# Performance work log

Measured on AMD Instinct MI355X. Metric: run time of the kernel, lower is better.

Reference implementation:

```python
import jax, jax.numpy as jnp
import numpy as np

B, N, D, H, KS, DQ = 2048, 20, 512, 8, 3, 64
DK = D // H
LN_EPS = 1e-5


def _conv1d_same(x_bdn, w_oik):
    # x: [B, D, N], w: [O, I, K] -> [B, O, N], 'same' padding
    return jax.lax.conv_general_dilated(
        x_bdn, w_oik, window_strides=(1,), padding='SAME',
        dimension_numbers=('NCH', 'OIH', 'NCH'))


def _layernorm(x, g, b):
    m = jnp.mean(x, axis=-1, keepdims=True)
    v = jnp.var(x, axis=-1, keepdims=True)
    return (x - m) * jax.lax.rsqrt(v + LN_EPS) * g + b


def setup_inputs() -> dict:
    key = jax.random.key(0)
    ks = jax.random.split(key, 12)
    s = 0.02
    inp = {
        'x': jax.random.normal(ks[0], (B, N, D), dtype=jnp.float32),
        'Wq': jax.random.normal(ks[1], (D, D, KS), dtype=jnp.float32) * s,
        'Wk': jax.random.normal(ks[2], (D, D, KS), dtype=jnp.float32) * s,
        'Wv': jax.random.normal(ks[3], (D, D, KS), dtype=jnp.float32) * s,
        'gq_g': jnp.ones((D,), jnp.float32), 'gq_b': jnp.zeros((D,), jnp.float32),
        'gk_g': jnp.ones((D,), jnp.float32), 'gk_b': jnp.zeros((D,), jnp.float32),
        'gv_g': jnp.ones((D,), jnp.float32), 'gv_b': jnp.zeros((D,), jnp.float32),
        'rel_table': jax.random.normal(ks[4], (2 * N - 1, H), dtype=jnp.float32) * s,
        'gsb': jax.random.normal(ks[5], (H, N, N), dtype=jnp.float32) * s,
        'alpha': jnp.asarray(1.0, jnp.float32),
        'Wqf': jax.random.normal(ks[6], (D, DQ), dtype=jnp.float32) * s,
        'bqf': jnp.zeros((DQ,), jnp.float32),
        'Wqp': jax.random.normal(ks[7], (DQ, H), dtype=jnp.float32) * s,
        'bqp': jnp.zeros((H,), jnp.float32),
        'Wo': jax.random.normal(ks[8], (D, D), dtype=jnp.float32) * s,
        'bo': jnp.zeros((D,), jnp.float32),
    }
    return inp


def reference(x, Wq, Wk, Wv, gq_g, gq_b, gk_g, gk_b, gv_g, gv_b,
              rel_table, gsb, alpha, Wqf, bqf, Wqp, bqp, Wo, bo):
    xp = jnp.transpose(x, (0, 2, 1))  # [B, D, N]
    # conv QKV projections + LayerNorm + residual (use_conv_proj=True path)
    q = x + _layernorm(jnp.transpose(_conv1d_same(xp, Wq), (0, 2, 1)), gq_g, gq_b)
    k = x + _layernorm(jnp.transpose(_conv1d_same(xp, Wk), (0, 2, 1)), gk_g, gk_b)
    v = x + _layernorm(jnp.transpose(_conv1d_same(xp, Wv), (0, 2, 1)), gv_g, gv_b)
    # split heads: [B, H, N, DK]
    q = q.reshape(B, N, H, DK).transpose(0, 2, 1, 3)
    k = k.reshape(B, N, H, DK).transpose(0, 2, 1, 3)
    v = v.reshape(B, N, H, DK).transpose(0, 2, 1, 3)
    scale = 1.0 / jnp.sqrt(jnp.asarray(DK, jnp.float32))
    scores = jnp.einsum('bhnd,bhmd->bhnm', q, k) * scale  # [B, H, N, N]
    # relative positional bias over node index
    idx = jnp.arange(N)[:, None] - jnp.arange(N)[None, :] + N - 1  # [N, N]
    rel_bias = rel_table[idx]  # [N, N, H]
    scores = scores + jnp.transpose(rel_bias, (2, 0, 1))[None]
    # learned global spatial bias
    scores = scores + alpha * gsb[None]
    # dynamic adjacency bias from pairwise node features
    qf = jnp.tanh(x @ Wqf + bqf)  # [B, N, DQ]
    pair = qf[:, :, None, :] - qf[:, None, :, :]  # [B, N, N, DQ]
    dyn = pair @ Wqp + bqp  # [B, N, N, H]
    scores = scores + jnp.transpose(dyn, (0, 3, 1, 2))
    attn = jax.nn.softmax(scores, axis=-1)
    out = jnp.einsum('bhnm,bhmd->bhnd', attn, v)
    out = out.transpose(0, 2, 1, 3).reshape(B, N, D)
    return out @ Wo + bo
```

## Files before the change

kernel.cpp:

```cpp
#include <hip/hip_runtime.h>
#include <stdint.h>

#define Bn   2048
#define Nn   20
#define Dn   512
#define Hn   8
#define Mn   (Bn*Nn)
#define K3n  1536
#define NPn  22
#define BKn  32

typedef __attribute__((ext_vector_type(4))) float  floatx4;
typedef __attribute__((ext_vector_type(8))) __bf16 bf16x8;
typedef __attribute__((ext_vector_type(4))) __bf16 bf16x4;

__device__ __forceinline__ void gload_lds16(const void* g, void* l) {
  __builtin_amdgcn_global_load_lds(
      (const __attribute__((address_space(1))) void*)g,
      (__attribute__((address_space(3))) void*)l, 16, 0, 0);
}

__global__ void k_prep_xpad(const float* __restrict__ x, __bf16* __restrict__ xpad) {
  int idx = blockIdx.x * 256 + threadIdx.x;
  int d8 = idx & 63;
  int t  = idx >> 6;
  if (t >= Bn * NPn) return;
  int n = t % NPn;
  int b = t / NPn;
  bf16x8 v;
  if (n == 0 || n == NPn - 1) {
#pragma unroll
    for (int e = 0; e < 8; ++e) v[e] = (__bf16)0.f;
  } else {
    const float4 x0 = *(const float4*)(x + (size_t)((b * Nn + n - 1) * Dn) + d8 * 8);
    const float4 x1 = *(const float4*)(x + (size_t)((b * Nn + n - 1) * Dn) + d8 * 8 + 4);
    v[0] = (__bf16)x0.x; v[1] = (__bf16)x0.y; v[2] = (__bf16)x0.z; v[3] = (__bf16)x0.w;
    v[4] = (__bf16)x1.x; v[5] = (__bf16)x1.y; v[6] = (__bf16)x1.z; v[7] = (__bf16)x1.w;
  }
  *(bf16x8*)(xpad + (size_t)t * Dn + d8 * 8) = v;
}

__global__ void k_prep_wctf(const float* __restrict__ Wq, const float* __restrict__ Wk,
                            const float* __restrict__ Wv, __bf16* __restrict__ wctf) {
  int t = blockIdx.x * 256 + threadIdx.x;
  if (t >= 48 * 96 * 64) return;
  int l  = t & 63;
  int cb = (t >> 6) % 96;
  int kt = t / (96 * 64);
  int col = cb * 16 + (l & 15);
  int k   = kt * 32 + (l >> 4) * 8;
  int seg = col >> 9, o = col & 511;
  int kker = k >> 9, i = k & 511;
  const float* W = (seg == 0) ? Wq : ((seg == 1) ? Wk : Wv);
  const float* s = W + ((size_t)o * 512 + i) * 3 + kker;
  bf16x8 v;
#pragma unroll
  for (int e = 0; e < 8; ++e) v[e] = (__bf16)s[e * 3];
  *(bf16x8*)(wctf + (size_t)t * 8) = v;
}

__global__ void k_prep_wotf(const float* __restrict__ Wo, __bf16* __restrict__ wotf) {
  int t = blockIdx.x * 256 + threadIdx.x;
  if (t >= 16 * 32 * 64) return;
  int l  = t & 63;
  int cb = (t >> 6) & 31;
  int kt = t / (32 * 64);
  int col = cb * 16 + (l & 15);
  int k   = kt * 32 + (l >> 4) * 8;
  const float* s = Wo + (size_t)k * 512 + col;
  bf16x8 v;
#pragma unroll
  for (int e = 0; e < 8; ++e) v[e] = (__bf16)s[(size_t)e * 512];
  *(bf16x8*)(wotf + (size_t)t * 8) = v;
}

__global__ void k_prep_wqft(const float* __restrict__ Wqf, __bf16* __restrict__ wqft) {
  int idx = blockIdx.x * 256 + threadIdx.x;
  if (idx >= Dn * 64) return;
  int d = idx & 511, dq = idx >> 9;
  wqft[idx] = (__bf16)Wqf[d * 64 + dq];
}

__global__ void k_bias(const float* __restrict__ rel, const float* __restrict__ gsb,
                       const float* __restrict__ alpha, const float* __restrict__ bqp,
                       float* __restrict__ bias) {
  int idx = blockIdx.x * 256 + threadIdx.x;
  if (idx >= Hn * Nn * Nn) return;
  int j = idx % Nn;
  int i = (idx / Nn) % Nn;
  int h = idx / (Nn * Nn);
  bias[idx] = rel[(i - j + Nn - 1) * Hn + h] + alpha[0] * gsb[idx] + bqp[h];
}

#define LOADB(DST, ADV) do {                                           \
    _Pragma("unroll")                                                  \
    for (int _tc = 0; _tc < 8; ++_tc)                                  \
      DST[_tc] = *(const bf16x8*)(gW + _tc * 512);                     \
    gW += (ADV);                                                       \
  } while (0)

#define STAGEA(NB) do {                                                \
    gload_lds16(gA0, myA + (NB) * 2048 +    0); gA0 += BKn;            \
    gload_lds16(gA1, myA + (NB) * 2048 +  512); gA1 += BKn;            \
    gload_lds16(gA2, myA + (NB) * 2048 + 1024); gA2 += BKn;            \
    gload_lds16(gA3, myA + (NB) * 2048 + 1536); gA3 += BKn;            \
  } while (0)

#define GSTEP(KT, CUR, NXT, CB, NB, LASTKT, ADV) do {                  \
    const __bf16* _L = myA + (CB) * 2048;                              \
    bf16x8 _a0 = *(const bf16x8*)(_L + fAo[0]);                        \
    bf16x8 _a1 = *(const bf16x8*)(_L + fAo[1]);                        \
    bf16x8 _a2 = *(const bf16x8*)(_L + fAo[2]);                        \
    bf16x8 _a3 = *(const bf16x8*)(_L + fAo[3]);                        \
    if ((KT) < (LASTKT)) { LOADB(NXT, ADV); STAGEA(NB); }              \
    __builtin_amdgcn_s_setprio(1);                                     \
    _Pragma("unroll")                                                  \
    for (int _tc = 0; _tc < 8; ++_tc) {                                \
      acc[0][_tc] = __builtin_amdgcn_mfma_f32_16x16x32_bf16(_a0, CUR[_tc], acc[0][_tc], 0, 0, 0); \
      acc[1][_tc] = __builtin_amdgcn_mfma_f32_16x16x32_bf16(_a1, CUR[_tc], acc[1][_tc], 0, 0, 0); \
      acc[2][_tc] = __builtin_amdgcn_mfma_f32_16x16x32_bf16(_a2, CUR[_tc], acc[2][_tc], 0, 0, 0); \
      acc[3][_tc] = __builtin_amdgcn_mfma_f32_16x16x32_bf16(_a3, CUR[_tc], acc[3][_tc], 0, 0, 0); \
    }                                                                  \
    __builtin_amdgcn_s_setprio(0);                                     \
    asm volatile("s_waitcnt vmcnt(0)" ::: "memory");                   \
  } while (0)

__global__ __launch_bounds__(256, 2)
void k_qkv(const __bf16* __restrict__ xpad, const __bf16* __restrict__ wctf,
           const float* __restrict__ gq_g, const float* __restrict__ gq_b,
           const float* __restrict__ gk_g, const float* __restrict__ gk_b,
           const float* __restrict__ gv_g, const float* __restrict__ gv_b,
           __bf16* __restrict__ qkv) {
  __shared__ __bf16 lA[4][2][2048];
  __shared__ float red1[256];
  __shared__ float red2[256];

  const int tid  = threadIdx.x;
  const int wv   = tid >> 6;
  const int lane = tid & 63;
  const int quad = lane >> 4;
  const int l15  = lane & 15;

  const int bid   = blockIdx.x;
  const int xcd   = bid & 7;
  const int local = bid >> 3;
  const int seg   = local / 80;
  const int mt    = xcd * 80 + (local % 80);
  const int m0    = mt * 64;

  const __bf16 *gA0, *gA1, *gA2, *gA3;
  {
    int c, row, rk, grow, b, n;
    c = 0 * 64 + lane; row = c >> 2; rk = (c & 3) ^ ((row >> 1) & 3);
    grow = m0 + row; b = grow / Nn; n = grow - b * Nn;
    gA0 = xpad + (size_t)(b * NPn + n) * Dn + rk * 8;
    c = 1 * 64 + lane; row = c >> 2; rk = (c & 3) ^ ((row >> 1) & 3);
    grow = m0 + row; b = grow / Nn; n = grow - b * Nn;
    gA1 = xpad + (size_t)(b * NPn + n) * Dn + rk * 8;
    c = 2 * 64 + lane; row = c >> 2; rk = (c & 3) ^ ((row >> 1) & 3);
    grow = m0 + row; b = grow / Nn; n = grow - b * Nn;
    gA2 = xpad + (size_t)(b * NPn + n) * Dn + rk * 8;
    c = 3 * 64 + lane; row = c >> 2; rk = (c & 3) ^ ((row >> 1) & 3);
    grow = m0 + row; b = grow / Nn; n = grow - b * Nn;
    gA3 = xpad + (size_t)(b * NPn + n) * Dn + rk * 8;
  }

  const __bf16* gW = wctf + ((size_t)(seg * 32 + wv * 8) * 512) + lane * 8;

  int fAo[4];
#pragma unroll
  for (int mi = 0; mi < 4; ++mi) {
    int row = mi * 16 + l15;
    fAo[mi] = row * BKn + (quad ^ ((row >> 1) & 3)) * 8;
  }
  __bf16* myA = &lA[wv][0][0];

  floatx4 acc[4][8];
  const floatx4 zero = {0.f, 0.f, 0.f, 0.f};
#pragma unroll
  for (int i = 0; i < 4; ++i)
#pragma unroll
    for (int j = 0; j < 8; ++j) acc[i][j] = zero;

  bf16x8 bA[8], bB[8];

  STAGEA(0);
  LOADB(bA, 49152);
  asm volatile("s_waitcnt vmcnt(0)" ::: "memory");

#pragma unroll 1
  for (int it = 0; it < 24; ++it) {
    GSTEP(2 * it,     bA, bB, 0, 1, 47, 49152);
    GSTEP(2 * it + 1, bB, bA, 1, 0, 47, 49152);
  }

  float s1[16], s2[16];
#pragma unroll
  for (int mi = 0; mi < 4; ++mi)
#pragma unroll
    for (int r = 0; r < 4; ++r) {
      float a = 0.f, b2 = 0.f;
#pragma unroll
      for (int tc = 0; tc < 8; ++tc) { float v = acc[mi][tc][r]; a += v; b2 += v * v; }
      s1[mi * 4 + r] = a; s2[mi * 4 + r] = b2;
    }
#pragma unroll
  for (int off = 1; off < 16; off <<= 1)
#pragma unroll
    for (int i = 0; i < 16; ++i) {
      s1[i] += __shfl_xor(s1[i], off, 64);
      s2[i] += __shfl_xor(s2[i], off, 64);
    }
  if (l15 == 0) {
#pragma unroll
    for (int i = 0; i < 16; ++i) {
      int mi = i >> 2, r = i & 3;
      int row = mi * 16 + quad * 4 + r;
      red1[row * 4 + wv] = s1[i];
      red2[row * 4 + wv] = s2[i];
    }
  }
  __syncthreads();

  const float* gg = (seg == 0) ? gq_g : ((seg == 1) ? gk_g : gv_g);
  const float* bb = (seg == 0) ? gq_b : ((seg == 1) ? gk_b : gv_b);
#pragma unroll
  for (int mi = 0; mi < 4; ++mi)
#pragma unroll
    for (int r = 0; r < 4; ++r) {
      int row = mi * 16 + quad * 4 + r;
      float su = red1[row * 4] + red1[row * 4 + 1] + red1[row * 4 + 2] + red1[row * 4 + 3];
      float sq = red2[row * 4] + red2[row * 4 + 1] + red2[row * 4 + 2] + red2[row * 4 + 3];
      float mn = su * (1.f / 512.f);
      float vv = sq * (1.f / 512.f) - mn * mn;
      float rstd = rsqrtf(vv + 1e-5f);
      int grow = m0 + row;
      int b = grow / Nn, n2 = grow - b * Nn;
      const __bf16* xr = xpad + (size_t)(b * NPn + n2 + 1) * Dn;
#pragma unroll
      for (int tc = 0; tc < 8; ++tc) {
        int col = wv * 128 + tc * 16 + l15;
        float val = (acc[mi][tc][r] - mn) * rstd * gg[col] + bb[col] + (float)xr[col];
        qkv[(size_t)grow * K3n + seg * 512 + col] = (__bf16)val;
      }
    }
}

__global__ __launch_bounds__(256)
void k_qfqp(const __bf16* __restrict__ xpad, const __bf16* __restrict__ wqft,
            const float* __restrict__ bqf, const float* __restrict__ wqp,
            float* __restrict__ qfp) {
  __shared__ __bf16 sA[64 * BKn];
  __shared__ __bf16 sB[64 * BKn];
  __shared__ float lWqpT[8 * 64];
  const int tid  = threadIdx.x;
  const int wave = tid >> 6;
  const int lane = tid & 63;
  const int quad = lane >> 4;
  const int l15  = lane & 15;
  const int m0   = blockIdx.x * 64;

#pragma unroll
  for (int t = tid; t < 512; t += 256) {
    int col = t & 63, h = t >> 6;
    lWqpT[t] = wqp[col * 8 + h];
  }

  int c = wave * 64 + lane;
  int rowc = c >> 2;
  int rk   = (c & 3) ^ ((rowc >> 1) & 3);
  int grow = m0 + rowc;
  int b = grow / Nn, n = grow - b * Nn;
  const __bf16* gA = xpad + (size_t)(b * NPn + n + 1) * Dn + rk * 8;
  const __bf16* gB = wqft + (size_t)rowc * Dn + rk * 8;

  int frow = wave * 16 + l15;
  const __bf16* fA = sA + frow * BKn + (quad ^ ((frow >> 1) & 3)) * 8;
  const __bf16* fB[4];
#pragma unroll
  for (int tc = 0; tc < 4; ++tc) {
    int col = tc * 16 + l15;
    fB[tc] = sB + col * BKn + (quad ^ ((col >> 1) & 3)) * 8;
  }

  const floatx4 zero = {0.f, 0.f, 0.f, 0.f};
  floatx4 acc[4] = {zero, zero, zero, zero};

  for (int kt = 0; kt < Dn / BKn; ++kt) {
    gload_lds16(gA, sA + wave * 512);
    gload_lds16(gB, sB + wave * 512);
    __syncthreads();
    bf16x8 a = *(const bf16x8*)fA;
#pragma unroll
    for (int tc = 0; tc < 4; ++tc)
      acc[tc] = __builtin_amdgcn_mfma_f32_16x16x32_bf16(a, *(const bf16x8*)fB[tc], acc[tc], 0, 0, 0);
    __syncthreads();
    gA += BKn; gB += BKn;
  }

  float part[4][8];
#pragma unroll
  for (int r = 0; r < 4; ++r)
#pragma unroll
    for (int h = 0; h < 8; ++h) part[r][h] = 0.f;
#pragma unroll
  for (int tc = 0; tc < 4; ++tc) {
    int col = tc * 16 + l15;
    float bq = bqf[col];
#pragma unroll
    for (int r = 0; r < 4; ++r) {
      float t = tanhf(acc[tc][r] + bq);
#pragma unroll
      for (int h = 0; h < 8; ++h) part[r][h] += t * lWqpT[h * 64 + col];
    }
  }
#pragma unroll
  for (int off = 1; off < 16; off <<= 1)
#pragma unroll
    for (int r = 0; r < 4; ++r)
#pragma unroll
      for (int h = 0; h < 8; ++h) part[r][h] += __shfl_xor(part[r][h], off, 64);
  if (l15 == 0) {
#pragma unroll
    for (int r = 0; r < 4; ++r) {
      int row = wave * 16 + quad * 4 + r;
#pragma unroll
      for (int h = 0; h < 8; ++h)
        qfp[(size_t)(m0 + row) * 8 + h] = part[r][h];
    }
  }
}

__global__ __launch_bounds__(256)
void k_attn(const __bf16* __restrict__ qkv, const float* __restrict__ qfp,
            const float* __restrict__ bias, __bf16* __restrict__ aout) {
  __shared__ float sq[4][Nn * 64];
  __shared__ float sk[4][Nn * 68];
  __shared__ float sv[4][Nn * 68];
  __shared__ float sp[4][Nn * Nn];
  __shared__ float sf[4][Nn];
  const int tid  = threadIdx.x;
  const int w    = tid >> 6;
  const int lane = tid & 63;
  const int p0 = blockIdx.x * 4 + w;
  const int b = p0 >> 3, h = p0 & 7;
  const __bf16* qb = qkv + (size_t)b * Nn * K3n + h * 64;

  for (int idx = lane; idx < 160; idx += 64) {
    int n = idx >> 3, c = (idx & 7) * 8;
    bf16x8 qv = *(const bf16x8*)(qb + (size_t)n * K3n + c);
    bf16x8 kv = *(const bf16x8*)(qb + (size_t)n * K3n + 512 + c);
    bf16x8 vv = *(const bf16x8*)(qb + (size_t)n * K3n + 1024 + c);
#pragma unroll
    for (int e = 0; e < 8; ++e) {
      sq[w][n * 64 + c + e] = (float)qv[e];
      sk[w][n * 68 + c + e] = (float)kv[e];
      sv[w][n * 68 + c + e] = (float)vv[e];
    }
  }
  if (lane < Nn) sf[w][lane] = qfp[(size_t)(b * Nn + lane) * 8 + h];
  __syncthreads();

  const float* bh = bias + h * Nn * Nn;
  for (int p = lane; p < Nn * Nn; p += 64) {
    int i = p / Nn, j = p - i * Nn;
    const float4* q4 = (const float4*)&sq[w][i * 64];
    const float4* k4 = (const float4*)&sk[w][j * 68];
    float s = 0.f;
#pragma unroll
    for (int d4 = 0; d4 < 16; ++d4) {
      float4 qa = q4[d4], ka = k4[d4];
      s += qa.x * ka.x + qa.y * ka.y + qa.z * ka.z + qa.w * ka.w;
    }
    sp[w][p] = s * 0.125f + bh[p] + sf[w][i] - sf[w][j];
  }
  __syncthreads();
  if (lane < Nn) {
    int i = lane;
    float* row = &sp[w][i * Nn];
    float mx = row[0];
    for (int j = 1; j < Nn; ++j) mx = fmaxf(mx, row[j]);
    float sum = 0.f;
    for (int j = 0; j < Nn; ++j) { float e = __expf(row[j] - mx); row[j] = e; sum += e; }
    float inv = 1.f / sum;
    for (int j = 0; j < Nn; ++j) row[j] *= inv;
  }
  __syncthreads();
  for (int i = 0; i < Nn; ++i) {
    float a = 0.f;
#pragma unroll
    for (int j = 0; j < Nn; ++j) a += sp[w][i * Nn + j] * sv[w][j * 68 + lane];
    aout[(size_t)(b * Nn + i) * Dn + h * 64 + lane] = (__bf16)a;
  }
}

__global__ __launch_bounds__(256, 2)
void k_oproj(const __bf16* __restrict__ aout, const __bf16* __restrict__ wotf,
             const float* __restrict__ bo, float* __restrict__ out) {
  __shared__ __bf16 lA[4][2][2048];
  const int tid  = threadIdx.x;
  const int wv   = tid >> 6;
  const int lane = tid & 63;
  const int quad = lane >> 4;
  const int l15  = lane & 15;

  const int bid = blockIdx.x;
  const int m0  = ((bid & 7) * 80 + (bid >> 3)) * 64;

  const __bf16 *gA0, *gA1, *gA2, *gA3;
  {
    int c, row, rk;
    c = 0 * 64 + lane; row = c >> 2; rk = (c & 3) ^ ((row >> 1) & 3);
    gA0 = aout + (size_t)(m0 + row) * Dn + rk * 8;
    c = 1 * 64 + lane; row = c >> 2; rk = (c & 3) ^ ((row >> 1) & 3);
    gA1 = aout + (size_t)(m0 + row) * Dn + rk * 8;
    c = 2 * 64 + lane; row = c >> 2; rk = (c & 3) ^ ((row >> 1) & 3);
    gA2 = aout + (size_t)(m0 + row) * Dn + rk * 8;
    c = 3 * 64 + lane; row = c >> 2; rk = (c & 3) ^ ((row >> 1) & 3);
    gA3 = aout + (size_t)(m0 + row) * Dn + rk * 8;
  }
  const __bf16* gW = wotf + ((size_t)(wv * 8) * 512) + lane * 8;

  int fAo[4];
#pragma unroll
  for (int mi = 0; mi < 4; ++mi) {
    int row = mi * 16 + l15;
    fAo[mi] = row * BKn + (quad ^ ((row >> 1) & 3)) * 8;
  }
  __bf16* myA = &lA[wv][0][0];

  floatx4 acc[4][8];
  const floatx4 zero = {0.f, 0.f, 0.f, 0.f};
#pragma unroll
  for (int i = 0; i < 4; ++i)
#pragma unroll
    for (int j = 0; j < 8; ++j) acc[i][j] = zero;

  bf16x8 bA[8], bB[8];

  STAGEA(0);
  LOADB(bA, 16384);
  asm volatile("s_waitcnt vmcnt(0)" ::: "memory");

#pragma unroll 1
  for (int it = 0; it < 8; ++it) {
    GSTEP(2 * it,     bA, bB, 0, 1, 15, 16384);
    GSTEP(2 * it + 1, bB, bA, 1, 0, 15, 16384);
  }

#pragma unroll
  for (int mi = 0; mi < 4; ++mi)
#pragma unroll
    for (int r = 0; r < 4; ++r) {
      int row = mi * 16 + quad * 4 + r;
#pragma unroll
      for (int tc = 0; tc < 8; ++tc) {
        int col = wv * 128 + tc * 16 + l15;
        out[(size_t)(m0 + row) * Dn + col] = acc[mi][tc][r] + bo[col];
      }
    }
}

static const size_t OFF_XPAD = 0;
static const size_t OFF_WCT  = 46137344;
static const size_t OFF_WOT  = 50855936;
static const size_t OFF_WQFT = 51380224;
static const size_t OFF_QKV  = 51445760;
static const size_t OFF_QFP  = 177274880;
static const size_t OFF_BIAS = 178585600;
static const size_t OFF_AOUT = 0;

extern "C" void kernel_launch(void* const* d_in, const int* in_sizes, int n_in,
                              void* d_out, int out_size, void* d_ws, size_t ws_size,
                              hipStream_t stream) {
  (void)in_sizes; (void)n_in; (void)out_size; (void)ws_size;
  const float* x     = (const float*)d_in[0];
  const float* Wq    = (const float*)d_in[1];
  const float* Wk    = (const float*)d_in[2];
  const float* Wv    = (const float*)d_in[3];
  const float* gq_g  = (const float*)d_in[4];
  const float* gq_b  = (const float*)d_in[5];
  const float* gk_g  = (const float*)d_in[6];
  const float* gk_b  = (const float*)d_in[7];
  const float* gv_g  = (const float*)d_in[8];
  const float* gv_b  = (const float*)d_in[9];
  const float* rel   = (const float*)d_in[10];
  const float* gsb   = (const float*)d_in[11];
  const float* alpha = (const float*)d_in[12];
  const float* Wqf   = (const float*)d_in[13];
  const float* bqf   = (const float*)d_in[14];
  const float* Wqp   = (const float*)d_in[15];
  const float* bqp   = (const float*)d_in[16];
  const float* Wo    = (const float*)d_in[17];
  const float* bo    = (const float*)d_in[18];
  float* out = (float*)d_out;
  char* ws = (char*)d_ws;

  __bf16* xpad = (__bf16*)(ws + OFF_XPAD);
  __bf16* wctf = (__bf16*)(ws + OFF_WCT);
  __bf16* wotf = (__bf16*)(ws + OFF_WOT);
  __bf16* wqft = (__bf16*)(ws + OFF_WQFT);
  __bf16* qkv  = (__bf16*)(ws + OFF_QKV);
  float*  qfp  = (float*)(ws + OFF_QFP);
  float*  bias = (float*)(ws + OFF_BIAS);
  __bf16* aout = (__bf16*)(ws + OFF_AOUT);

  k_prep_xpad<<<(Bn * NPn * (Dn / 8) + 255) / 256, 256, 0, stream>>>(x, xpad);
  k_prep_wctf<<<(48 * 96 * 64 + 255) / 256, 256, 0, stream>>>(Wq, Wk, Wv, wctf);
  k_prep_wotf<<<(16 * 32 * 64 + 255) / 256, 256, 0, stream>>>(Wo, wotf);
  k_prep_wqft<<<(Dn * 64 + 255) / 256, 256, 0, stream>>>(Wqf, wqft);
  k_bias     <<<(Hn * Nn * Nn + 255) / 256, 256, 0, stream>>>(rel, gsb, alpha, bqp, bias);

  k_qkv <<<Mn / 64 * 3, 256, 0, stream>>>(xpad, wctf, gq_g, gq_b, gk_g, gk_b, gv_g, gv_b, qkv);
  k_qfqp<<<Mn / 64, 256, 0, stream>>>(xpad, wqft, bqf, Wqp, qfp);
  k_attn<<<(Bn * Hn) / 4, 256, 0, stream>>>(qkv, qfp, bias, aout);
  k_oproj<<<Mn / 64, 256, 0, stream>>>(aout, wotf, bo, out);
}
```

Before: 569.7 us.

## Share A tile across 8 waves with 128-row blocks in QKV and output GEMMs

Moves the QKV and output-projection GEMMs from 256-thread blocks with per-wave private 64-row A tiles to 512-thread blocks of 128 rows. All 8 waves now share one LDS A tile, and each wave computes 128 rows by 64 columns. The aim is to cut redundant A loads and raise reuse of the B fragments held in registers. The cost is a block-wide s_barrier every k-step, which the old per-wave pipeline avoided. Block-to-segment mapping also interleaves q/k/v segments per row tile.

```diff
diff --git a/kernel.cpp b/kernel.cpp
--- a/kernel.cpp
+++ b/kernel.cpp
@@ -92,48 +92,50 @@
   bias[idx] = rel[(i - j + Nn - 1) * Hn + h] + alpha[0] * gsb[idx] + bqp[h];
 }
 
-#define LOADB(DST, ADV) do {                                           \
+#define LOADB4(DST, ADV) do {                                          \
     _Pragma("unroll")                                                  \
-    for (int _tc = 0; _tc < 8; ++_tc)                                  \
+    for (int _tc = 0; _tc < 4; ++_tc)                                  \
       DST[_tc] = *(const bf16x8*)(gW + _tc * 512);                     \
     gW += (ADV);                                                       \
   } while (0)
 
-#define STAGEA(NB) do {                                                \
-    gload_lds16(gA0, myA + (NB) * 2048 +    0); gA0 += BKn;            \
-    gload_lds16(gA1, myA + (NB) * 2048 +  512); gA1 += BKn;            \
-    gload_lds16(gA2, myA + (NB) * 2048 + 1024); gA2 += BKn;            \
-    gload_lds16(gA3, myA + (NB) * 2048 + 1536); gA3 += BKn;            \
-  } while (0)
-
-#define GSTEP(KT, CUR, NXT, CB, NB, LASTKT, ADV) do {                  \
-    const __bf16* _L = myA + (CB) * 2048;                              \
+#define QSTEP(CB, NB, CUR, NXT, DOSTAGE, ADV) do {                     \
+    if (DOSTAGE) {                                                     \
+      gload_lds16(gA, lsA + (NB) * 4096 + dA); gA += BKn;              \
+      LOADB4(NXT, ADV);                                                \
+    }                                                                  \
+    const __bf16* _L = lsA + (CB) * 4096;                              \
     bf16x8 _a0 = *(const bf16x8*)(_L + fAo[0]);                        \
     bf16x8 _a1 = *(const bf16x8*)(_L + fAo[1]);                        \
     bf16x8 _a2 = *(const bf16x8*)(_L + fAo[2]);                        \
     bf16x8 _a3 = *(const bf16x8*)(_L + fAo[3]);                        \
-    if ((KT) < (LASTKT)) { LOADB(NXT, ADV); STAGEA(NB); }              \
+    bf16x8 _a4 = *(const bf16x8*)(_L + fAo[4]);                        \
+    bf16x8 _a5 = *(const bf16x8*)(_L + fAo[5]);                        \
+    bf16x8 _a6 = *(const bf16x8*)(_L + fAo[6]);                        \
+    bf16x8 _a7 = *(const bf16x8*)(_L + fAo[7]);                        \
     __builtin_amdgcn_s_setprio(1);                                     \
     _Pragma("unroll")                                                  \
-    for (int _tc = 0; _tc < 8; ++_tc) {                                \
+    for (int _tc = 0; _tc < 4; ++_tc) {                                \
       acc[0][_tc] = __builtin_amdgcn_mfma_f32_16x16x32_bf16(_a0, CUR[_tc], acc[0][_tc], 0, 0, 0); \
       acc[1][_tc] = __builtin_amdgcn_mfma_f32_16x16x32_bf16(_a1, CUR[_tc], acc[1][_tc], 0, 0, 0); \
       acc[2][_tc] = __builtin_amdgcn_mfma_f32_16x16x32_bf16(_a2, CUR[_tc], acc[2][_tc], 0, 0, 0); \
       acc[3][_tc] = __builtin_amdgcn_mfma_f32_16x16x32_bf16(_a3, CUR[_tc], acc[3][_tc], 0, 0, 0); \
+      acc[4][_tc] = __builtin_amdgcn_mfma_f32_16x16x32_bf16(_a4, CUR[_tc], acc[4][_tc], 0, 0, 0); \
+      acc[5][_tc] = __builtin_amdgcn_mfma_f32_16x16x32_bf16(_a5, CUR[_tc], acc[5][_tc], 0, 0, 0); \
+      acc[6][_tc] = __builtin_amdgcn_mfma_f32_16x16x32_bf16(_a6, CUR[_tc], acc[6][_tc], 0, 0, 0); \
+      acc[7][_tc] = __builtin_amdgcn_mfma_f32_16x16x32_bf16(_a7, CUR[_tc], acc[7][_tc], 0, 0, 0); \
     }                                                                  \
     __builtin_amdgcn_s_setprio(0);                                     \
-    asm volatile("s_waitcnt vmcnt(0)" ::: "memory");                   \
+    asm volatile("s_waitcnt vmcnt(0) lgkmcnt(0)\n\ts_barrier" ::: "memory"); \
   } while (0)
 
-__global__ __launch_bounds__(256, 2)
+__global__ __launch_bounds__(512, 2)
 void k_qkv(const __bf16* __restrict__ xpad, const __bf16* __restrict__ wctf,
            const float* __restrict__ gq_g, const float* __restrict__ gq_b,
            const float* __restrict__ gk_g, const float* __restrict__ gk_b,
            const float* __restrict__ gv_g, const float* __restrict__ gv_b,
            __bf16* __restrict__ qkv) {
-  __shared__ __bf16 lA[4][2][2048];
-  __shared__ float red1[256];
-  __shared__ float red2[256];
+  __shared__ __bf16 lsA[2 * 4096];
 
   const int tid  = threadIdx.x;
   const int wv   = tid >> 6;
@@ -144,93 +146,81 @@
   const int bid   = blockIdx.x;
   const int xcd   = bid & 7;
   const int local = bid >> 3;
-  const int seg   = local / 80;
-  const int mt    = xcd * 80 + (local % 80);
-  const int m0    = mt * 64;
-
-  const __bf16 *gA0, *gA1, *gA2, *gA3;
+  const int seg   = local % 3;
+  const int mt    = xcd * 40 + local / 3;
+  const int m0    = mt * 128;
+
+  const __bf16* gA;
   {
-    int c, row, rk, grow, b, n;
-    c = 0 * 64 + lane; row = c >> 2; rk = (c & 3) ^ ((row >> 1) & 3);
-    grow = m0 + row; b = grow / Nn; n = grow - b * Nn;
-    gA0 = xpad + (size_t)(b * NPn + n) * Dn + rk * 8;
-    c = 1 * 64 + lane; row = c >> 2; rk = (c & 3) ^ ((row >> 1) & 3);
-    grow = m0 + row; b = grow / Nn; n = grow - b * Nn;
-    gA1 = xpad + (size_t)(b * NPn + n) * Dn + rk * 8;
-    c = 2 * 64 + lane; row = c >> 2; rk = (c & 3) ^ ((row >> 1) & 3);
-    grow = m0 + row; b = grow / Nn; n = grow - b * Nn;
-    gA2 = xpad + (size_t)(b * NPn + n) * Dn + rk * 8;
-    c = 3 * 64 + lane; row = c >> 2; rk = (c & 3) ^ ((row >> 1) & 3);
-    grow = m0 + row; b = grow / Nn; n = grow - b * Nn;
-    gA3 = xpad + (size_t)(b * NPn + n) * Dn + rk * 8;
-  }
-
-  const __bf16* gW = wctf + ((size_t)(seg * 32 + wv * 8) * 512) + lane * 8;
-
-  int fAo[4];
-#pragma unroll
-  for (int mi = 0; mi < 4; ++mi) {
+    int c   = tid;
+    int row = c >> 2;
+    int rk  = (c & 3) ^ ((row >> 1) & 3);
+    int grow = m0 + row;
+    int b = grow / Nn, n = grow - b * Nn;
+    gA = xpad + (size_t)(b * NPn + n) * Dn + rk * 8;
+  }
+  const int dA = wv * 512;
+
+  const __bf16* gW = wctf + ((size_t)(seg * 32 + wv * 4) * 512) + lane * 8;
+
+  int fAo[8];
+#pragma unroll
+  for (int mi = 0; mi < 8; ++mi) {
     int row = mi * 16 + l15;
     fAo[mi] = row * BKn + (quad ^ ((row >> 1) & 3)) * 8;
   }
-  __bf16* myA = &lA[wv][0][0];
-
-  floatx4 acc[4][8];
+
+  floatx4 acc[8][4];
   const floatx4 zero = {0.f, 0.f, 0.f, 0.f};
 #pragma unroll
-  for (int i = 0; i < 4; ++i)
-#pragma unroll
-    for (int j = 0; j < 8; ++j) acc[i][j] = zero;
-
-  bf16x8 bA[8], bB[8];
-
-  STAGEA(0);
-  LOADB(bA, 49152);
-  asm volatile("s_waitcnt vmcnt(0)" ::: "memory");
+  for (int i = 0; i < 8; ++i)
+#pragma unroll
+    for (int j = 0; j < 4; ++j) acc[i][j] = zero;
+
+  bf16x8 bA[4], bB[4];
+
+  gload_lds16(gA, lsA + dA); gA += BKn;
+  LOADB4(bA, 49152);
+  asm volatile("s_waitcnt vmcnt(0)\n\ts_barrier" ::: "memory");
 
 #pragma unroll 1
   for (int it = 0; it < 24; ++it) {
-    GSTEP(2 * it,     bA, bB, 0, 1, 47, 49152);
-    GSTEP(2 * it + 1, bB, bA, 1, 0, 47, 49152);
-  }
-
-  float s1[16], s2[16];
-#pragma unroll
-  for (int mi = 0; mi < 4; ++mi)
+    QSTEP(0, 1, bA, bB, (2 * it)     < 47, 49152);
+    QSTEP(1, 0, bB, bA, (2 * it + 1) < 47, 49152);
+  }
+
+  float* red1 = (float*)lsA;
+  float* red2 = red1 + 1024;
+#pragma unroll
+  for (int mi = 0; mi < 8; ++mi)
 #pragma unroll
     for (int r = 0; r < 4; ++r) {
       float a = 0.f, b2 = 0.f;
 #pragma unroll
-      for (int tc = 0; tc < 8; ++tc) { float v = acc[mi][tc][r]; a += v; b2 += v * v; }
-      s1[mi * 4 + r] = a; s2[mi * 4 + r] = b2;
-    }
-#pragma unroll
-  for (int off = 1; off < 16; off <<= 1)
-#pragma unroll
-    for (int i = 0; i < 16; ++i) {
-      s1[i] += __shfl_xor(s1[i], off, 64);
-      s2[i] += __shfl_xor(s2[i], off, 64);
-    }
-  if (l15 == 0) {
-#pragma unroll
-    for (int i = 0; i < 16; ++i) {
-      int mi = i >> 2, r = i & 3;
-      int row = mi * 16 + quad * 4 + r;
-      red1[row * 4 + wv] = s1[i];
-      red2[row * 4 + wv] = s2[i];
-    }
-  }
+      for (int tc = 0; tc < 4; ++tc) { float v = acc[mi][tc][r]; a += v; b2 += v * v; }
+#pragma unroll
+      for (int off = 1; off < 16; off <<= 1) {
+        a  += __shfl_xor(a, off, 64);
+        b2 += __shfl_xor(b2, off, 64);
+      }
+      if (l15 == 0) {
+        int row = mi * 16 + quad * 4 + r;
+        red1[row * 8 + wv] = a;
+        red2[row * 8 + wv] = b2;
+      }
+    }
   __syncthreads();
 
   const float* gg = (seg == 0) ? gq_g : ((seg == 1) ? gk_g : gv_g);
   const float* bb = (seg == 0) ? gq_b : ((seg == 1) ? gk_b : gv_b);
 #pragma unroll
-  for (int mi = 0; mi < 4; ++mi)
+  for (int mi = 0; mi < 8; ++mi)
 #pragma unroll
     for (int r = 0; r < 4; ++r) {
       int row = mi * 16 + quad * 4 + r;
-      float su = red1[row * 4] + red1[row * 4 + 1] + red1[row * 4 + 2] + red1[row * 4 + 3];
-      float sq = red2[row * 4] + red2[row * 4 + 1] + red2[row * 4 + 2] + red2[row * 4 + 3];
+      float su = 0.f, sq = 0.f;
+#pragma unroll
+      for (int w = 0; w < 8; ++w) { su += red1[row * 8 + w]; sq += red2[row * 8 + w]; }
       float mn = su * (1.f / 512.f);
       float vv = sq * (1.f / 512.f) - mn * mn;
       float rstd = rsqrtf(vv + 1e-5f);
@@ -238,8 +228,8 @@
       int b = grow / Nn, n2 = grow - b * Nn;
       const __bf16* xr = xpad + (size_t)(b * NPn + n2 + 1) * Dn;
 #pragma unroll
-      for (int tc = 0; tc < 8; ++tc) {
-        int col = wv * 128 + tc * 16 + l15;
+      for (int tc = 0; tc < 4; ++tc) {
+        int col = wv * 64 + tc * 16 + l15;
         float val = (acc[mi][tc][r] - mn) * rstd * gg[col] + bb[col] + (float)xr[col];
         qkv[(size_t)grow * K3n + seg * 512 + col] = (__bf16)val;
       }
@@ -394,10 +384,10 @@
   }
 }
 
-__global__ __launch_bounds__(256, 2)
+__global__ __launch_bounds__(512, 2)
 void k_oproj(const __bf16* __restrict__ aout, const __bf16* __restrict__ wotf,
              const float* __restrict__ bo, float* __restrict__ out) {
-  __shared__ __bf16 lA[4][2][2048];
+  __shared__ __bf16 lsA[2 * 4096];
   const int tid  = threadIdx.x;
   const int wv   = tid >> 6;
   const int lane = tid & 63;
@@ -405,57 +395,52 @@
   const int l15  = lane & 15;
 
   const int bid = blockIdx.x;
-  const int m0  = ((bid & 7) * 80 + (bid >> 3)) * 64;
-
-  const __bf16 *gA0, *gA1, *gA2, *gA3;
+  const int m0  = ((bid & 7) * 40 + (bid >> 3)) * 128;
+
+  const __bf16* gA;
   {
-    int c, row, rk;
-    c = 0 * 64 + lane; row = c >> 2; rk = (c & 3) ^ ((row >> 1) & 3);
-    gA0 = aout + (size_t)(m0 + row) * Dn + rk * 8;
-    c = 1 * 64 + lane; row = c >> 2; rk = (c & 3) ^ ((row >> 1) & 3);
-    gA1 = aout + (size_t)(m0 + row) * Dn + rk * 8;
-    c = 2 * 64 + lane; row = c >> 2; rk = (c & 3) ^ ((row >> 1) & 3);
-    gA2 = aout + (size_t)(m0 + row) * Dn + rk * 8;
-    c = 3 * 64 + lane; row = c >> 2; rk = (c & 3) ^ ((row >> 1) & 3);
-    gA3 = aout + (size_t)(m0 + row) * Dn + rk * 8;
-  }
-  const __bf16* gW = wotf + ((size_t)(wv * 8) * 512) + lane * 8;
-
-  int fAo[4];
-#pragma unroll
-  for (int mi = 0; mi < 4; ++mi) {
+    int c   = tid;
+    int row = c >> 2;
+    int rk  = (c & 3) ^ ((row >> 1) & 3);
+    gA = aout + (size_t)(m0 + row) * Dn + rk * 8;
+  }
+  const int dA = wv * 512;
+  const __bf16* gW = wotf + ((size_t)(wv * 4) * 512) + lane * 8;
+
+  int fAo[8];
+#pragma unroll
+  for (int mi = 0; mi < 8; ++mi) {
     int row = mi * 16 + l15;
     fAo[mi] = row * BKn + (quad ^ ((row >> 1) & 3)) * 8;
   }
-  __bf16* myA = &lA[wv][0][0];
-
-  floatx4 acc[4][8];
+
+  floatx4 acc[8][4];
   const floatx4 zero = {0.f, 0.f, 0.f, 0.f};
 #pragma unroll
-  for (int i = 0; i < 4; ++i)
-#pragma unroll
-    for (int j = 0; j < 8; ++j) acc[i][j] = zero;
-
-  bf16x8 bA[8], bB[8];
-
-  STAGEA(0);
-  LOADB(bA, 16384);
-  asm volatile("s_waitcnt vmcnt(0)" ::: "memory");
+  for (int i = 0; i < 8; ++i)
+#pragma unroll
+    for (int j = 0; j < 4; ++j) acc[i][j] = zero;
+
+  bf16x8 bA[4], bB[4];
+
+  gload_lds16(gA, lsA + dA); gA += BKn;
+  LOADB4(bA, 16384);
+  asm volatile("s_waitcnt vmcnt(0)\n\ts_barrier" ::: "memory");
 
 #pragma unroll 1
   for (int it = 0; it < 8; ++it) {
-    GSTEP(2 * it,     bA, bB, 0, 1, 15, 16384);
-    GSTEP(2 * it + 1, bB, bA, 1, 0, 15, 16384);
-  }
-
-#pragma unroll
-  for (int mi = 0; mi < 4; ++mi)
+    QSTEP(0, 1, bA, bB, (2 * it)     < 15, 16384);
+    QSTEP(1, 0, bB, bA, (2 * it + 1) < 15, 16384);
+  }
+
+#pragma unroll
+  for (int mi = 0; mi < 8; ++mi)
 #pragma unroll
     for (int r = 0; r < 4; ++r) {
       int row = mi * 16 + quad * 4 + r;
 #pragma unroll
-      for (int tc = 0; tc < 8; ++tc) {
-        int col = wv * 128 + tc * 16 + l15;
+      for (int tc = 0; tc < 4; ++tc) {
+        int col = wv * 64 + tc * 16 + l15;
         out[(size_t)(m0 + row) * Dn + col] = acc[mi][tc][r] + bo[col];
       }
     }
@@ -511,8 +496,8 @@
   k_prep_wqft<<<(Dn * 64 + 255) / 256, 256, 0, stream>>>(Wqf, wqft);
   k_bias     <<<(Hn * Nn * Nn + 255) / 256, 256, 0, stream>>>(rel, gsb, alpha, bqp, bias);
 
-  k_qkv <<<Mn / 64 * 3, 256, 0, stream>>>(xpad, wctf, gq_g, gq_b, gk_g, gk_b, gv_g, gv_b, qkv);
+  k_qkv <<<Mn / 128 * 3, 512, 0, stream>>>(xpad, wctf, gq_g, gq_b, gk_g, gk_b, gv_g, gv_b, qkv);
   k_qfqp<<<Mn / 64, 256, 0, stream>>>(xpad, wqft, bqf, Wqp, qfp);
   k_attn<<<(Bn * Hn) / 4, 256, 0, stream>>>(qkv, qfp, bias, aout);
-  k_oproj<<<Mn / 64, 256, 0, stream>>>(aout, wotf, bo, out);
-}
+  k_oproj<<<Mn / 128, 512, 0, stream>>>(aout, wotf, bo, out);
+}
```

After: 575.8 us. About the same (+1.1%).
